# Optimization experiments

Measured on AMD Instinct MI355X. Metric: run time of the kernel, lower is better.

## Reference

```python
import jax, jax.numpy as jnp
import numpy as np

EPS = 1e-6
AREA_WIDTH = 3
NHEAD = 8
DIM = 16


def _skew(v):
    # v: [N,3] -> [N,3,3] cross-product matrix
    x, y, z = v[..., 0], v[..., 1], v[..., 2]
    zero = jnp.zeros_like(x)
    return jnp.stack([
        jnp.stack([zero, -z, y], -1),
        jnp.stack([z, zero, -x], -1),
        jnp.stack([-y, x, zero], -1)], -2)


def _create_meshgrid(h, w):
    # kornia create_meshgrid(..., normalized=False): last dim is (x, y), row-major flatten
    xs = jnp.arange(w, dtype=jnp.float32)
    ys = jnp.arange(h, dtype=jnp.float32)
    gx, gy = jnp.meshgrid(xs, ys, indexing='xy')  # [h,w]
    return jnp.stack([gx, gy], -1).reshape(h * w, 2)  # [S,2]


def _epipolar_lines(coord, R, t, K0, K1):
    # coord [S,2]; R [N,3,3]; t [N,3,1] -> lines [N,S,3] (unit-normalized a,b), mode [N,S]
    S = coord.shape[0]
    p = jnp.concatenate([coord, jnp.ones((S, 1), coord.dtype)], -1)  # [S,3]
    E = _skew(t[..., 0]) @ R                                         # [t]_x R
    F = jnp.swapaxes(jnp.linalg.inv(K1), -1, -2) @ E @ jnp.linalg.inv(K0)
    lines = jnp.einsum('nij,sj->nsi', F, p)
    n = jnp.linalg.norm(lines[..., :2], axis=-1, keepdims=True)
    lines = lines / jnp.maximum(n, 1e-12)
    mode = jnp.abs(lines[..., 1]) >= jnp.abs(lines[..., 0])  # True: solve y(x) (|b|>=|a|)
    return lines, mode


def _get_mask(lines, mode, coord, area_width):
    # lines [N,L,3], mode [N,L], coord [S,2] -> within [N,L,S]
    a, b, c = lines[..., 0], lines[..., 1], lines[..., 2]
    xs, ys = coord[:, 0], coord[:, 1]
    hw = area_width / 2.0
    safe = lambda d: jnp.where(jnp.abs(d) < 1e-12, 1e-12, d)
    cy = (-a / safe(b))[..., None] * xs + (-c / safe(b))[..., None]  # [N,L,S]
    cx = (-b / safe(a))[..., None] * ys + (-c / safe(a))[..., None]
    wy = (ys < cy + hw) & (ys > cy - hw)
    wx = (xs < cx + hw) & (xs > cx - hw)
    return jnp.where(mode[..., None], wy, wx)


def _gather_index(within, C):
    # sort-based top-C compaction, index 0 doubles as padding (faithful to source)
    S = within.shape[-1]
    idx = jnp.arange(S, dtype=jnp.int32)
    ti = jnp.where(within, idx[None, None, :], 0)
    ti = jnp.sort(ti, axis=-1)[..., -C:]
    return ti, ti != 0


def _feature_map(x):
    return jax.nn.elu(x) + 1.0


def reference(queries, keys, values, solved_sample, K0, K1, R, t, h0c, w0c, scale):
    N, L, H, D = queries.shape
    sol = np.asarray(solved_sample).astype(bool)  # static split of the batch
    sol_idx = np.nonzero(sol)[0]
    uns_idx = np.nonzero(~sol)[0]
    Q = _feature_map(queries)
    K = _feature_map(keys)
    out = jnp.zeros((N, L, H, D), queries.dtype)

    if sol_idx.size > 0:  # epipolar-gathered candidate attention, direction '0to1'
        coord = _create_meshgrid(h0c, w0c)
        K0s = K0[sol_idx].at[:, :2, :].mul(1.0 / scale)
        K1s = K1[sol_idx].at[:, :2, :].mul(1.0 / scale)
        C = max(h0c, w0c) * AREA_WIDTH
        lines, mode = _epipolar_lines(coord, R[sol_idx], t[sol_idx], K0s, K1s)
        within = _get_mask(lines, mode, coord, AREA_WIDTH)       # [Ns,L,S]
        index, mask = _gather_index(within, C)                    # [Ns,L,C]
        Ns = sol_idx.size
        n_ix = jnp.arange(Ns)[:, None, None]
        Qs = Q[sol_idx]
        Ks = K[sol_idx][n_ix, index]            # [Ns,L,C,H,D]
        Vs = values[sol_idx][n_ix, index]
        m = mask[..., None, None].astype(Ks.dtype)
        Ks = Ks * m
        Vs = Vs * m / C
        KV = jnp.einsum('nlchd,nlchv->nlhdv', Ks, Vs)
        Z = 1.0 / (jnp.einsum('nlhd,nlhd->nlh', Qs, Ks.sum(2)) + EPS)
        out = out.at[sol_idx].set(jnp.einsum('nlhd,nlhdv,nlh->nlhv', Qs, KV, Z) * C)

    if uns_idx.size > 0:  # plain linear attention
        Qu, Ku, Vu = Q[uns_idx], K[uns_idx], values[uns_idx]
        S = Ku.shape[1]
        KV = jnp.einsum('nshd,nshv->nhdv', Ku, Vu / S)
        Z = 1.0 / (jnp.einsum('nlhd,nhd->nlh', Qu, Ku.sum(1)) + EPS)
        out = out.at[uns_idx].set(jnp.einsum('nlhd,nhdv,nlh->nlhv', Qu, KV, Z) * S)
    return out


def setup_inputs() -> dict:
    key = jax.random.key(0)
    kq, kk, kv = jax.random.split(key, 3)
    N, H, D = 4, NHEAD, DIM
    h0c, w0c = 48, 64
    L = h0c * w0c
    queries = jax.random.normal(kq, (N, L, H, D), jnp.float32)
    keys = jax.random.normal(kk, (N, L, H, D), jnp.float32)
    values = jax.random.normal(kv, (N, L, H, D), jnp.float32)
    solved_sample = jnp.array([True, True, False, False])
    Kmat = np.array([[600., 0., 256.], [0., 600., 192.], [0., 0., 1.]], np.float32)
    K0 = jnp.asarray(np.tile(Kmat, (N, 1, 1)))
    Rl, tl = [], []
    for i in range(N):
        th = 0.05 * (i + 1)
        Rl.append(np.array([[np.cos(th), 0., np.sin(th)], [0., 1., 0.],
                            [-np.sin(th), 0., np.cos(th)]], np.float32))
        tl.append(np.array([[0.2 + 0.01 * i], [0.05], [0.02]], np.float32))
    R = jnp.asarray(np.stack(Rl))
    t = jnp.asarray(np.stack(tl))
    return {"queries": queries, "keys": keys, "values": values,
            "solved_sample": solved_sample, "K0": K0, "K1": K0, "R": R, "t": t,
            "h0c": h0c, "w0c": w0c, "scale": 8}
```

## Files before the change

kernel.cpp:

```cpp
#include <hip/hip_runtime.h>
#include <math.h>

#define NHEAD 8
#define DIM   16
#define EPSF  1e-6f
#define KVCH  8

typedef _Float16 half2_t __attribute__((ext_vector_type(2)));
typedef _Float16 half4_t __attribute__((ext_vector_type(4)));
typedef _Float16 half8_t __attribute__((ext_vector_type(8)));

#if defined(__has_builtin)
#if __has_builtin(__builtin_amdgcn_fdot2)
#define HAVE_FDOT2 1
#endif
#endif

__device__ __forceinline__ float dot2(half2_t a, half2_t b, float c) {
#ifdef HAVE_FDOT2
    return __builtin_amdgcn_fdot2(a, b, c, false);
#else
    return c + (float)a.x * (float)b.x + (float)a.y * (float)b.y;
#endif
}

__device__ __forceinline__ bool solved_flag(const void* p, int i) {
    const unsigned int* u = (const unsigned int*)p;
    unsigned int v0 = u[0];
    if (v0 <= 1u)             return u[i] != 0u;
    if (v0 == 0x3F800000u)    return ((const float*)p)[i] != 0.0f;
    return ((const unsigned char*)p)[i] != 0;
}

__device__ __forceinline__ float fm(float x) {
    return x > 0.f ? x + 1.f : expf(x);
}

__device__ void inv3d(const double* M, double* inv) {
    double det = M[0]*(M[4]*M[8]-M[5]*M[7]) - M[1]*(M[3]*M[8]-M[5]*M[6]) + M[2]*(M[3]*M[7]-M[4]*M[6]);
    double id = 1.0 / det;
    inv[0] =  (M[4]*M[8]-M[5]*M[7])*id;
    inv[1] = -(M[1]*M[8]-M[2]*M[7])*id;
    inv[2] =  (M[1]*M[5]-M[2]*M[4])*id;
    inv[3] = -(M[3]*M[8]-M[5]*M[6])*id;
    inv[4] =  (M[0]*M[8]-M[2]*M[6])*id;
    inv[5] = -(M[0]*M[5]-M[2]*M[3])*id;
    inv[6] =  (M[3]*M[7]-M[4]*M[6])*id;
    inv[7] = -(M[0]*M[7]-M[1]*M[6])*id;
    inv[8] =  (M[0]*M[4]-M[1]*M[3])*id;
}

__device__ void compute_F_one(const float* K0, const float* K1, const float* R,
                              const float* t, float invs, float* Fout, int n) {
    double A[9], B[9];
    for (int i = 0; i < 9; ++i) {
        float a = K0[n*9 + i], b = K1[n*9 + i];
        if (i < 6) { a *= invs; b *= invs; }
        A[i] = (double)a; B[i] = (double)b;
    }
    double iA[9], iB[9];
    inv3d(A, iA); inv3d(B, iB);
    double tx = t[n*3+0], ty = t[n*3+1], tz = t[n*3+2];
    double S[9] = {0.0,-tz,ty, tz,0.0,-tx, -ty,tx,0.0};
    double E[9], M[9];
    for (int i = 0; i < 3; ++i)
        for (int j = 0; j < 3; ++j) {
            double s = 0.0;
            for (int k = 0; k < 3; ++k) s += S[i*3+k] * (double)R[n*9 + k*3 + j];
            E[i*3+j] = s;
        }
    for (int i = 0; i < 3; ++i)
        for (int j = 0; j < 3; ++j) {
            double s = 0.0;
            for (int k = 0; k < 3; ++k) s += E[i*3+k] * iA[k*3+j];
            M[i*3+j] = s;
        }
    for (int i = 0; i < 3; ++i)
        for (int j = 0; j < 3; ++j) {
            double s = 0.0;
            for (int k = 0; k < 3; ++k) s += iB[k*3+i] * M[k*3+j];
            Fout[n*9 + i*3 + j] = (float)s;
        }
}

__launch_bounds__(256)
__global__ void prep_kv(const float4* __restrict__ Kr4, const float4* __restrict__ Vr4,
                        _Float16* __restrict__ Kh, _Float16* __restrict__ Vh, int n4,
                        const float* __restrict__ Kr, const float* __restrict__ Vr,
                        const void* __restrict__ flags,
                        float* __restrict__ KVp, float* __restrict__ Ksp,
                        const float* __restrict__ K0, const float* __restrict__ K1,
                        const float* __restrict__ R,  const float* __restrict__ t,
                        const int* __restrict__ scale_p, float* __restrict__ Fout,
                        int N, int L, int PB) {
    if ((int)blockIdx.x < PB) {
        int i = blockIdx.x * 256 + threadIdx.x;
        if (i < n4) {
            float4 k = Kr4[i];
            half4_t kh = { (_Float16)fm(k.x), (_Float16)fm(k.y), (_Float16)fm(k.z), (_Float16)fm(k.w) };
            ((half4_t*)Kh)[i] = kh;
            float4 v = Vr4[i];
            half4_t vh = { (_Float16)v.x, (_Float16)v.y, (_Float16)v.z, (_Float16)v.w };
            ((half4_t*)Vh)[i] = vh;
        }
        if (blockIdx.x == 0 && threadIdx.x < (unsigned)N) {
            float invs = 1.0f / (float)(*scale_p);
            compute_F_one(K0, K1, R, t, invs, Fout, threadIdx.x);
        }
    } else {
        int kb = blockIdx.x - PB;
        int chunk = kb & (KVCH - 1);
        int h = (kb >> 3) & 7;
        int n = kb >> 6;
        if (n >= N || solved_flag(flags, n)) return;
        int tdx = threadIdx.x;
        int d = tdx >> 4, v = tdx & 15;
        int rowsPer = (L + KVCH - 1) / KVCH;
        int r0 = chunk * rowsPer;
        int r1 = min(r0 + rowsPer, L);
        const float* Kb = Kr + (size_t)n * L * (NHEAD * DIM) + h * DIM;
        const float* Vb = Vr + (size_t)n * L * (NHEAD * DIM) + h * DIM;
        float acc = 0.f, ks = 0.f;
        #pragma unroll 8
        for (int s = r0; s < r1; ++s) {
            float kd = fm(Kb[(size_t)s * (NHEAD * DIM) + d]);
            float vv = Vb[(size_t)s * (NHEAD * DIM) + v];
            acc += kd * vv;
            ks  += kd;
        }
        KVp[(((size_t)chunk * N + n) * NHEAD + h) * 256 + (d << 4) + v] = acc;
        if (v == 0) Ksp[(((size_t)chunk * N + n) * NHEAD + h) * 16 + d] = ks;
    }
}

__launch_bounds__(256)
__global__ void mega(const float* __restrict__ Qr,
                     const _Float16* __restrict__ Kh, const _Float16* __restrict__ Vh,
                     const void* __restrict__ flags,  const float* __restrict__ F,
                     const float* __restrict__ KVp,   const float* __restrict__ Ksp,
                     float* __restrict__ outp,
                     const int* __restrict__ h0c_p, const int* __restrict__ w0c_p,
                     int N, int L, int Bs) {
    if ((int)blockIdx.x < Bs) {
        int wid = (blockIdx.x << 2) | (threadIdx.x >> 6);
        wid = __builtin_amdgcn_readfirstlane(wid);
        int lane = threadIdx.x & 63;
        int n = wid / L;
        if (n >= N) return;
        if (!solved_flag(flags, n)) return;
        int s = wid - n * L;
        int W  = *w0c_p;
        int Hc = *h0c_p;
        float px = (float)(s % W);
        float py = (float)(s / W);

        const float* Fn = F + n * 9;
        float a = Fn[0]*px + Fn[1]*py + Fn[2];
        float b = Fn[3]*px + Fn[4]*py + Fn[5];
        float c = Fn[6]*px + Fn[7]*py + Fn[8];
        float nrm = sqrtf(a*a + b*b);
        float mdiv = fmaxf(nrm, 1e-12f);
        a /= mdiv; b /= mdiv; c /= mdiv;
        bool mode = fabsf(b) >= fabsf(a);

        float slope, inter;
        int outerN, innerMax, sI, sO;
        if (mode) {
            float bs = (fabsf(b) < 1e-12f) ? 1e-12f : b;
            slope = -a / bs; inter = -c / bs;
            outerN = W; innerMax = Hc; sI = W; sO = 1;
        } else {
            float as = (fabsf(a) < 1e-12f) ? 1e-12f : a;
            slope = -b / as; inter = -c / as;
            outerN = Hc; innerMax = W; sI = 1; sO = W;
        }

        int c8 = lane >> 3;
        int h  = lane & 7;

        const float4* q4 = (const float4*)(Qr + (size_t)wid * (NHEAD * DIM) + h * DIM);
        half2_t q2[8];
        {
            float4 a0 = q4[0], a1 = q4[1], a2 = q4[2], a3 = q4[3];
            q2[0] = (half2_t){ (_Float16)fm(a0.x), (_Float16)fm(a0.y) };
            q2[1] = (half2_t){ (_Float16)fm(a0.z), (_Float16)fm(a0.w) };
            q2[2] = (half2_t){ (_Float16)fm(a1.x), (_Float16)fm(a1.y) };
            q2[3] = (half2_t){ (_Float16)fm(a1.z), (_Float16)fm(a1.w) };
            q2[4] = (half2_t){ (_Float16)fm(a2.x), (_Float16)fm(a2.y) };
            q2[5] = (half2_t){ (_Float16)fm(a2.z), (_Float16)fm(a2.w) };
            q2[6] = (half2_t){ (_Float16)fm(a3.x), (_Float16)fm(a3.y) };
            q2[7] = (half2_t){ (_Float16)fm(a3.z), (_Float16)fm(a3.w) };
        }

        const _Float16* Kb = Kh + (size_t)n * L * (NHEAD * DIM);
        const _Float16* Vb = Vh + (size_t)n * L * (NHEAD * DIM);

        half2_t acc2[8];
        #pragma unroll
        for (int i = 0; i < 8; ++i) acc2[i] = (half2_t){ (_Float16)0.f, (_Float16)0.f };
        float den = 0.f;

        int totalC = outerN * 3;
        int groups = (totalC + 7) >> 3;
        const float hw = 1.5f;

        #pragma unroll 2
        for (int g = 0; g < groups; ++g) {
            int m = (g << 3) + c8;
            int o = (int)((unsigned)m / 3u);
            int j = m - o * 3;
            float cc = fmaf(slope, (float)o, inter);
            float lo = cc - hw, hi = cc + hw;
            int ii = (int)floorf(lo) + 1 + j;
            float fi = (float)ii;
            bool valid = (m < totalC) && (ii >= 0) && (ii < innerMax)
                         && (fi > lo) && (fi < hi);
            int s2 = ii * sI + o * sO;
            valid = valid && (s2 != 0);
            int idx = ((valid ? s2 : 0) << 7) + (h << 4);
            const half8_t* kr = (const half8_t*)(Kb + idx);
            const half8_t* vr = (const half8_t*)(Vb + idx);
            half8_t k0 = kr[0], k1 = kr[1];
            half8_t v0 = vr[0], v1 = vr[1];
            union H8 { half8_t v; half2_t h[4]; };
            H8 ku0, ku1, vu0, vu1;
            ku0.v = k0; ku1.v = k1; vu0.v = v0; vu1.v = v1;
            float sA = 0.f, sB = 0.f;
            sA = dot2(q2[0], ku0.h[0], sA);
            sB = dot2(q2[1], ku0.h[1], sB);
            sA = dot2(q2[2], ku0.h[2], sA);
            sB = dot2(q2[3], ku0.h[3], sB);
            sA = dot2(q2[4], ku1.h[0], sA);
            sB = dot2(q2[5], ku1.h[1], sB);
            sA = dot2(q2[6], ku1.h[2], sA);
            sB = dot2(q2[7], ku1.h[3], sB);
            float sc = sA + sB;
            sc = valid ? sc : 0.f;
            den += sc;
            _Float16 sch = (_Float16)sc;
            half2_t scv = (half2_t){ sch, sch };
            acc2[0] += scv * vu0.h[0];
            acc2[1] += scv * vu0.h[1];
            acc2[2] += scv * vu0.h[2];
            acc2[3] += scv * vu0.h[3];
            acc2[4] += scv * vu1.h[0];
            acc2[5] += scv * vu1.h[1];
            acc2[6] += scv * vu1.h[2];
            acc2[7] += scv * vu1.h[3];
        }

        den += __shfl_xor(den, 8);
        den += __shfl_xor(den, 16);
        den += __shfl_xor(den, 32);

        bool hi8 = (lane & 8) != 0;
        half2_t t4[4];
        #pragma unroll
        for (int j2 = 0; j2 < 4; ++j2) {
            half2_t send = hi8 ? acc2[j2] : acc2[4 + j2];
            int rr = __shfl_xor(__builtin_bit_cast(int, send), 8);
            half2_t keep = hi8 ? acc2[4 + j2] : acc2[j2];
            t4[j2] = keep + __builtin_bit_cast(half2_t, rr);
        }
        bool hi16 = (lane & 16) != 0;
        half2_t t2[2];
        #pragma unroll
        for (int j2 = 0; j2 < 2; ++j2) {
            half2_t send = hi16 ? t4[j2] : t4[2 + j2];
            int rr = __shfl_xor(__builtin_bit_cast(int, send), 16);
            half2_t keep = hi16 ? t4[2 + j2] : t4[j2];
            t2[j2] = keep + __builtin_bit_cast(half2_t, rr);
        }
        bool hi32 = (lane & 32) != 0;
        half2_t t1;
        {
            half2_t send = hi32 ? t2[0] : t2[1];
            int rr = __shfl_xor(__builtin_bit_cast(int, send), 32);
            half2_t keep = hi32 ? t2[1] : t2[0];
            t1 = keep + __builtin_bit_cast(half2_t, rr);
        }
        int e0 = (hi8 ? 8 : 0) + (hi16 ? 4 : 0) + (hi32 ? 2 : 0);
        float r = 1.0f / (den + EPSF);
        float2 o2 = { (float)t1.x * r, (float)t1.y * r };
        *(float2*)(outp + (size_t)wid * (NHEAD * DIM) + h * DIM + e0) = o2;
    } else {
        long long tot2 = (long long)N * L * NHEAD * DIM / 2;
        long long idx2 = (long long)(blockIdx.x - Bs) * 256 + threadIdx.x;
        if (idx2 >= tot2) return;
        int p = (int)(idx2 & 63);
        int h = p >> 3;
        int v = (p & 7) * 2;
        long long ns = idx2 >> 6;
        int n = (int)(ns / L);
        if (solved_flag(flags, n)) return;
        const float* qrow = Qr + ns * (NHEAD * DIM) + h * DIM;
        float num0 = 0.f, num1 = 0.f, den = 0.f;
        #pragma unroll
        for (int d = 0; d < 16; ++d) {
            float qd = fm(qrow[d]);
            #pragma unroll
            for (int cch = 0; cch < KVCH; ++cch) {
                const float2 kv2 = *(const float2*)(KVp + (((size_t)cch * N + n) * NHEAD + h) * 256 + (d << 4) + v);
                num0 += qd * kv2.x;
                num1 += qd * kv2.y;
                den  += qd * Ksp[(((size_t)cch * N + n) * NHEAD + h) * 16 + d] * (1.0f / 16.0f);
            }
        }
        den *= 16.0f;
        float rdiv = 1.0f / (den + EPSF);
        size_t ob = ns * (NHEAD * DIM) + h * DIM + v;
        outp[ob]     = num0 * rdiv;
        outp[ob + 1] = num1 * rdiv;
    }
}

extern "C" void kernel_launch(void* const* d_in, const int* in_sizes, int n_in,
                              void* d_out, int out_size, void* d_ws, size_t ws_size,
                              hipStream_t stream) {
    const float* Qr   = (const float*)d_in[0];
    const float* Kr   = (const float*)d_in[1];
    const float* Vr   = (const float*)d_in[2];
    const void*  flag = d_in[3];
    const float* K0   = (const float*)d_in[4];
    const float* K1   = (const float*)d_in[5];
    const float* R    = (const float*)d_in[6];
    const float* t    = (const float*)d_in[7];
    const int*   h0c  = (const int*)d_in[8];
    const int*   w0c  = (const int*)d_in[9];
    const int*   scl  = (const int*)d_in[10];

    int N = in_sizes[3];
    int T = in_sizes[0];
    int L = T / (N * NHEAD * DIM);

    _Float16* Kh = (_Float16*)d_ws;
    _Float16* Vh = Kh + T;
    float* Fm   = (float*)(Vh + T);
    float* KVp  = Fm + (size_t)N * 9;
    float* Ksp  = KVp + (size_t)KVCH * N * NHEAD * 256;

    float* outp = (float*)d_out;

    int n4 = T / 4;
    int PB = (n4 + 255) / 256;
    int KB = N * NHEAD * KVCH;
    prep_kv<<<PB + KB, 256, 0, stream>>>((const float4*)Kr, (const float4*)Vr,
                                         Kh, Vh, n4, Kr, Vr, flag, KVp, Ksp,
                                         K0, K1, R, t, scl, Fm, N, L, PB);

    int Bs = (N * L + 3) / 4;
    long long tot2 = (long long)N * L * NHEAD * DIM / 2;
    int Bu = (int)((tot2 + 255) / 256);
    mega<<<Bs + Bu, 256, 0, stream>>>(Qr, Kh, Vh, flag, Fm, KVp, Ksp, outp,
                                      h0c, w0c, N, L, Bs);
}
```

Baseline: 173.3 us.

## Split each query's epipolar gather across two waves with an LDS index table

In the solved-sample path, each query's candidate pixels are now split between two wavefronts instead of one. Each wave first precomputes its gather offsets into a shared-memory table, and invalid entries point to an appended zero row in the half-precision K/V buffers, so the per-iteration validity select disappears. The two waves' partial numerators and denominators are merged through LDS before the output is written. This halves the serial gather chain per query and hoists index arithmetic out of the hot loop, at the cost of extra block-level barriers, more blocks, and a workspace layout change.

```diff
diff --git a/kernel.cpp b/kernel.cpp
--- a/kernel.cpp
+++ b/kernel.cpp
@@ -103,9 +103,17 @@
             half4_t vh = { (_Float16)v.x, (_Float16)v.y, (_Float16)v.z, (_Float16)v.w };
             ((half4_t*)Vh)[i] = vh;
         }
-        if (blockIdx.x == 0 && threadIdx.x < (unsigned)N) {
-            float invs = 1.0f / (float)(*scale_p);
-            compute_F_one(K0, K1, R, t, invs, Fout, threadIdx.x);
+        if (blockIdx.x == 0) {
+            if (threadIdx.x < (unsigned)N) {
+                float invs = 1.0f / (float)(*scale_p);
+                compute_F_one(K0, K1, R, t, invs, Fout, threadIdx.x);
+            }
+            if (threadIdx.x >= 64 && threadIdx.x < 192) {
+                int tz = threadIdx.x - 64;
+                size_t zr = (size_t)N * L * 128 + tz;
+                Kh[zr] = (_Float16)0.f;
+                Vh[zr] = (_Float16)0.f;
+            }
         }
     } else {
         int kb = blockIdx.x - PB;
@@ -141,14 +149,20 @@
                      float* __restrict__ outp,
                      const int* __restrict__ h0c_p, const int* __restrict__ w0c_p,
                      int N, int L, int Bs) {
+    __shared__ int    tbl[4][96];
+    __shared__ float2 comb[2][64];
+    __shared__ float  dcomb[2][8];
     if ((int)blockIdx.x < Bs) {
-        int wid = (blockIdx.x << 2) | (threadIdx.x >> 6);
-        wid = __builtin_amdgcn_readfirstlane(wid);
+        int w    = threadIdx.x >> 6;
+        int p    = w & 1;
+        int qp   = w >> 1;
         int lane = threadIdx.x & 63;
-        int n = wid / L;
+        int q    = blockIdx.x * 2 + qp;
+        int n    = q / L;
         if (n >= N) return;
         if (!solved_flag(flags, n)) return;
-        int s = wid - n * L;
+        int NL = N * L;
+        int s = q - n * L;
         int W  = *w0c_p;
         int Hc = *h0c_p;
         float px = (float)(s % W);
@@ -177,8 +191,9 @@
 
         int c8 = lane >> 3;
         int h  = lane & 7;
-
-        const float4* q4 = (const float4*)(Qr + (size_t)wid * (NHEAD * DIM) + h * DIM);
+        int h16 = h << 4;
+
+        const float4* q4 = (const float4*)(Qr + (size_t)q * (NHEAD * DIM) + h16);
         half2_t q2[8];
         {
             float4 a0 = q4[0], a1 = q4[1], a2 = q4[2], a3 = q4[3];
@@ -192,21 +207,12 @@
             q2[7] = (half2_t){ (_Float16)fm(a3.z), (_Float16)fm(a3.w) };
         }
 
-        const _Float16* Kb = Kh + (size_t)n * L * (NHEAD * DIM);
-        const _Float16* Vb = Vh + (size_t)n * L * (NHEAD * DIM);
-
-        half2_t acc2[8];
-        #pragma unroll
-        for (int i = 0; i < 8; ++i) acc2[i] = (half2_t){ (_Float16)0.f, (_Float16)0.f };
-        float den = 0.f;
-
         int totalC = outerN * 3;
-        int groups = (totalC + 7) >> 3;
+        int zsent  = NL << 7;
         const float hw = 1.5f;
-
-        #pragma unroll 2
-        for (int g = 0; g < groups; ++g) {
-            int m = (g << 3) + c8;
+        for (int tt = lane; tt < 96; tt += 64) {
+            int g = tt >> 3, c8t = tt & 7;
+            int m = (g << 4) | (p << 3) | c8t;
             int o = (int)((unsigned)m / 3u);
             int j = m - o * 3;
             float cc = fmaf(slope, (float)o, inter);
@@ -217,9 +223,21 @@
                          && (fi > lo) && (fi < hi);
             int s2 = ii * sI + o * sO;
             valid = valid && (s2 != 0);
-            int idx = ((valid ? s2 : 0) << 7) + (h << 4);
-            const half8_t* kr = (const half8_t*)(Kb + idx);
-            const half8_t* vr = (const half8_t*)(Vb + idx);
+            tbl[w][tt] = valid ? ((n * L + s2) << 7) : zsent;
+        }
+        __syncthreads();
+
+        half2_t acc2[8];
+        #pragma unroll
+        for (int i = 0; i < 8; ++i) acc2[i] = (half2_t){ (_Float16)0.f, (_Float16)0.f };
+        float den = 0.f;
+
+        int groups = (totalC + 15) >> 4;
+        #pragma unroll 3
+        for (int g = 0; g < groups; ++g) {
+            int entry = tbl[w][(g << 3) + c8];
+            const half8_t* kr = (const half8_t*)(Kh + entry + h16);
+            const half8_t* vr = (const half8_t*)(Vh + entry + h16);
             half8_t k0 = kr[0], k1 = kr[1];
             half8_t v0 = vr[0], v1 = vr[1];
             union H8 { half8_t v; half2_t h[4]; };
@@ -235,7 +253,6 @@
             sA = dot2(q2[6], ku1.h[2], sA);
             sB = dot2(q2[7], ku1.h[3], sB);
             float sc = sA + sB;
-            sc = valid ? sc : 0.f;
             den += sc;
             _Float16 sch = (_Float16)sc;
             half2_t scv = (half2_t){ sch, sch };
@@ -280,16 +297,26 @@
             t1 = keep + __builtin_bit_cast(half2_t, rr);
         }
         int e0 = (hi8 ? 8 : 0) + (hi16 ? 4 : 0) + (hi32 ? 2 : 0);
-        float r = 1.0f / (den + EPSF);
-        float2 o2 = { (float)t1.x * r, (float)t1.y * r };
-        *(float2*)(outp + (size_t)wid * (NHEAD * DIM) + h * DIM + e0) = o2;
+
+        if (p == 1) {
+            comb[qp][lane] = make_float2((float)t1.x, (float)t1.y);
+            if (lane < 8) dcomb[qp][lane] = den;
+        }
+        __syncthreads();
+        if (p == 0) {
+            float2 oth = comb[qp][lane];
+            float dtot = den + dcomb[qp][h];
+            float r = 1.0f / (dtot + EPSF);
+            float2 o2 = { ((float)t1.x + oth.x) * r, ((float)t1.y + oth.y) * r };
+            *(float2*)(outp + (size_t)q * (NHEAD * DIM) + h16 + e0) = o2;
+        }
     } else {
         long long tot2 = (long long)N * L * NHEAD * DIM / 2;
         long long idx2 = (long long)(blockIdx.x - Bs) * 256 + threadIdx.x;
         if (idx2 >= tot2) return;
-        int p = (int)(idx2 & 63);
-        int h = p >> 3;
-        int v = (p & 7) * 2;
+        int pp = (int)(idx2 & 63);
+        int h = pp >> 3;
+        int v = (pp & 7) * 2;
         long long ns = idx2 >> 6;
         int n = (int)(ns / L);
         if (solved_flag(flags, n)) return;
@@ -303,10 +330,9 @@
                 const float2 kv2 = *(const float2*)(KVp + (((size_t)cch * N + n) * NHEAD + h) * 256 + (d << 4) + v);
                 num0 += qd * kv2.x;
                 num1 += qd * kv2.y;
-                den  += qd * Ksp[(((size_t)cch * N + n) * NHEAD + h) * 16 + d] * (1.0f / 16.0f);
+                den  += qd * Ksp[(((size_t)cch * N + n) * NHEAD + h) * 16 + d];
             }
         }
-        den *= 16.0f;
         float rdiv = 1.0f / (den + EPSF);
         size_t ob = ns * (NHEAD * DIM) + h * DIM + v;
         outp[ob]     = num0 * rdiv;
@@ -333,9 +359,10 @@
     int T = in_sizes[0];
     int L = T / (N * NHEAD * DIM);
 
+    size_t arr = (size_t)T + 8 * 128;
     _Float16* Kh = (_Float16*)d_ws;
-    _Float16* Vh = Kh + T;
-    float* Fm   = (float*)(Vh + T);
+    _Float16* Vh = Kh + arr;
+    float* Fm   = (float*)(Vh + arr);
     float* KVp  = Fm + (size_t)N * 9;
     float* Ksp  = KVp + (size_t)KVCH * N * NHEAD * 256;
 
@@ -348,7 +375,7 @@
                                          Kh, Vh, n4, Kr, Vr, flag, KVp, Ksp,
                                          K0, K1, R, t, scl, Fm, N, L, PB);
 
-    int Bs = (N * L + 3) / 4;
+    int Bs = (N * L) / 2;
     long long tot2 = (long long)N * L * NHEAD * DIM / 2;
     int Bu = (int)((tot2 + 255) / 256);
     mega<<<Bs + Bu, 256, 0, stream>>>(Qr, Kh, Vh, flag, Fm, KVp, Ksp, outp,
```

Measured after the change: 178.5 us. 3.0% more time.
